# Optimization experiments

Measured on AMD Instinct MI355X. Metric: run time of the kernel, lower is better.

Reference implementation:

```python
import jax, jax.numpy as jnp
import numpy as np

B, N, F_IN, F_OUT, D = 8, 2048, 256, 128, 3
ALPHA = 0.2       # leaky relu slope
CUT_OFF = 0.1     # distance gate sharpness
NEG_INF = -9e15


def setup_inputs() -> dict:
    key = jax.random.key(0)
    k1, k2, k3, k4 = jax.random.split(key, 4)
    x = jax.random.normal(k1, (B, N, F_IN), dtype=jnp.float32)
    coord = jax.random.normal(k2, (B, N, D), dtype=jnp.float32)
    # xavier_uniform-style scale (gain=1.414); normal init is fine for a reference
    w_std = 1.414 * np.sqrt(2.0 / (F_IN + F_OUT))
    a_std = 1.414 * np.sqrt(2.0 / (2 * F_OUT + 1))
    W = jax.random.normal(k3, (F_IN, F_OUT), dtype=jnp.float32) * w_std
    a = jax.random.normal(k4, (2 * F_OUT, 1), dtype=jnp.float32) * a_std
    return {"x": x, "coord": coord, "W": W, "a": a}


def reference(x, coord, W, a):
    # h: [B, N, F_OUT]
    h = jnp.matmul(x, W)
    # The original builds a_input=[h_i || h_j] and does a_input @ a.
    # Equivalent: e_ij = leaky_relu(h_i @ a[:F] + h_j @ a[F:]).
    f_src = jnp.matmul(h, a[:F_OUT])   # [B, N, 1]
    f_dst = jnp.matmul(h, a[F_OUT:])   # [B, N, 1]
    e = f_src + jnp.swapaxes(f_dst, 1, 2)            # [B, N, N]
    e = jnp.where(e > 0, e, ALPHA * e)               # leaky relu
    # pairwise squared distances -> exponential gate
    diff = coord[:, :, None, :] - coord[:, None, :, :]   # [B, N, N, D]
    loc = jnp.exp(-CUT_OFF * jnp.sum(diff * diff, axis=-1))  # [B, N, N]
    att_logits = jnp.where(loc > 0.01, e * loc, NEG_INF)
    attention = jax.nn.softmax(att_logits, axis=2)
    # dropout is identity in eval mode
    h_prime = jnp.matmul(attention, h)               # [B, N, F_OUT]
    return jax.nn.elu(h_prime)                       # concat=True path
```

## Files before the change

kernel.cpp:

```cpp
#include <hip/hip_runtime.h>
#include <hip/hip_bf16.h>

#define B_    8
#define N_    2048
#define FIN_  256
#define FOUT_ 128
#define NROWS (B_*N_)

typedef __attribute__((ext_vector_type(8))) short short8;
typedef __attribute__((ext_vector_type(4))) float f32x4;

__device__ __forceinline__ float bf2f(unsigned short u) {
  return __uint_as_float(((unsigned int)u) << 16);
}
__device__ __forceinline__ unsigned short f2bf(float f) {
  unsigned int u = __float_as_uint(f);
  u += 0x7FFFu + ((u >> 16) & 1u);
  return (unsigned short)(u >> 16);
}
__device__ __forceinline__ float ldin(const void* p, size_t idx, int isbf) {
  if (isbf) return bf2f(((const unsigned short*)p)[idx]);
  return ((const float*)p)[idx];
}
__device__ __forceinline__ unsigned pk2bf(float a, float b) {
  return (unsigned)f2bf(a) | ((unsigned)f2bf(b) << 16);
}
__device__ __forceinline__ float ex2(float x) {
#if __has_builtin(__builtin_amdgcn_exp2f)
  return __builtin_amdgcn_exp2f(x);
#else
  return __expf(x * 0.69314718056f);
#endif
}
__device__ __forceinline__ unsigned encf(float f) {
  unsigned u = __float_as_uint(f);
  return (u & 0x80000000u) ? ~u : (u | 0x80000000u);
}
__device__ __forceinline__ float decf(unsigned k) {
  return (k & 0x80000000u) ? __uint_as_float(k ^ 0x80000000u) : __uint_as_float(~k);
}
__device__ __forceinline__ int detect_bf(const void* x, int* cnt) {
  const unsigned short* u = (const unsigned short*)x;
  int c = 0;
  for (int i = threadIdx.x; i < 8192; i += 256) {
    unsigned short v = u[i];
    int e = (v >> 7) & 0xFF;
    if ((e >= 110 && e <= 145) || (v & 0x7FFF) == 0) c++;
  }
  cnt[threadIdx.x] = c;
  __syncthreads();
  for (int s = 128; s > 0; s >>= 1) {
    if (threadIdx.x < s) cnt[threadIdx.x] += cnt[threadIdx.x + s];
    __syncthreads();
  }
  return cnt[0] > 7373;
}

__global__ __launch_bounds__(256)
void k_prep(const void* __restrict__ x, const void* __restrict__ W,
            const void* __restrict__ a,
            unsigned short* __restrict__ WT, float* __restrict__ wa,
            int* __restrict__ flag, unsigned* __restrict__ MdstE) {
  __shared__ int cnt[256];
  const int isbf = detect_bf(x, cnt);
  if (blockIdx.x < 128) {
    int f = blockIdx.x, k = threadIdx.x;
    WT[f * 256 + k] = f2bf(ldin(W, (size_t)k * 128 + f, isbf));
  } else {
    __shared__ float as_s[256];
    int k = threadIdx.x;
    as_s[k] = ldin(a, k, isbf);
    __syncthreads();
    float s = 0.f, d = 0.f;
    for (int f = 0; f < 128; f++) {
      float w = ldin(W, (size_t)k * 128 + f, isbf);
      s += w * as_s[f];
      d += w * as_s[128 + f];
    }
    wa[k] = s;
    wa[256 + k] = d;
    if (k == 0) *flag = isbf;
    if (k < 8) MdstE[k * 32] = 0u;
  }
}

__global__ __launch_bounds__(256)
void k_h(const void* __restrict__ x, const void* __restrict__ coord,
         const unsigned short* __restrict__ WT,
         const float* __restrict__ wa, const int* __restrict__ flag,
         unsigned short* __restrict__ hT, float* __restrict__ fsrc,
         float4* __restrict__ cpack, unsigned* __restrict__ MdstE) {
  __shared__ __align__(16) unsigned short xs[32][264];
  __shared__ float wa_s[512];
  __shared__ float mxs[8];
  const int isbf = *flag;
  const int t    = threadIdx.x;
  const int row0 = blockIdx.x * 32;

  wa_s[t] = wa[t];
  wa_s[256 + t] = wa[256 + t];
  __syncthreads();

  const int c = t & 31;
  float sp[4], dp[4];
  if (isbf) {
    const unsigned short* xu = (const unsigned short*)x;
#pragma unroll
    for (int u = 0; u < 4; u++) {
      int r = u * 8 + (t >> 5);
      short8 sh = *(const short8*)&xu[(size_t)(row0 + r) * FIN_ + c * 8];
      *(short8*)&xs[r][c * 8] = sh;
      float s = 0.f, d = 0.f;
#pragma unroll
      for (int e = 0; e < 8; e++) {
        float xv = bf2f((unsigned short)sh[e]);
        s += xv * wa_s[c * 8 + e];
        d += xv * wa_s[256 + c * 8 + e];
      }
      sp[u] = s; dp[u] = d;
    }
  } else {
    const float* xf = (const float*)x;
#pragma unroll
    for (int u = 0; u < 4; u++) {
      int r = u * 8 + (t >> 5);
      float4 v0 = *(const float4*)&xf[(size_t)(row0 + r) * FIN_ + c * 8];
      float4 v1 = *(const float4*)&xf[(size_t)(row0 + r) * FIN_ + c * 8 + 4];
      float vv[8] = {v0.x, v0.y, v0.z, v0.w, v1.x, v1.y, v1.z, v1.w};
      short8 sh;
      float s = 0.f, d = 0.f;
#pragma unroll
      for (int e = 0; e < 8; e++) {
        sh[e] = (short)f2bf(vv[e]);
        s += vv[e] * wa_s[c * 8 + e];
        d += vv[e] * wa_s[256 + c * 8 + e];
      }
      *(short8*)&xs[r][c * 8] = sh;
      sp[u] = s; dp[u] = d;
    }
  }
#pragma unroll
  for (int off = 16; off >= 1; off >>= 1) {
#pragma unroll
    for (int u = 0; u < 4; u++) {
      sp[u] += __shfl_xor(sp[u], off, 64);
      dp[u] += __shfl_xor(dp[u], off, 64);
    }
  }
  if (c == 0) {
    float lm = -1e30f;
#pragma unroll
    for (int u = 0; u < 4; u++) {
      int r = u * 8 + (t >> 5);
      size_t rg = (size_t)(row0 + r);
      fsrc[rg] = sp[u];
      cpack[rg] = make_float4(ldin(coord, rg * 3 + 0, isbf),
                              ldin(coord, rg * 3 + 1, isbf),
                              ldin(coord, rg * 3 + 2, isbf),
                              dp[u] * 1.44269504f);
      lm = fmaxf(lm, dp[u]);
    }
    mxs[t >> 5] = lm;
  }
  __syncthreads();
  if (t == 0) {
    float m8 = mxs[0];
#pragma unroll
    for (int i = 1; i < 8; i++) m8 = fmaxf(m8, mxs[i]);
    atomicMax(&MdstE[(row0 >> 11) * 32], encf(m8));
  }

  const int lane = t & 63, w = t >> 6;
  const int m = lane & 15, quad = lane >> 4;
  const int slab = w >> 1, fh = w & 1;

  f32x4 acc[4];
#pragma unroll
  for (int i = 0; i < 4; i++) acc[i] = (f32x4){0.f, 0.f, 0.f, 0.f};

#pragma unroll
  for (int ks = 0; ks < 8; ks++) {
    short8 ah = *(const short8*)&xs[slab * 16 + m][ks * 32 + quad * 8];
#pragma unroll
    for (int ft = 0; ft < 4; ft++) {
      int f = fh * 64 + ft * 16 + m;
      short8 bh = *(const short8*)&WT[(size_t)f * 256 + ks * 32 + quad * 8];
      acc[ft] = __builtin_amdgcn_mfma_f32_16x16x32_bf16(ah, bh, acc[ft], 0, 0, 0);
    }
  }

  size_t n0 = (size_t)blockIdx.x * 2 + slab;
  unsigned short* hblk = hT + n0 * (FOUT_ * 16);
#pragma unroll
  for (int ft = 0; ft < 4; ft++) {
    int f = fh * 64 + ft * 16 + m;
    *(uint2*)&hblk[f * 16 + quad * 4] = make_uint2(
        pk2bf(acc[ft][0], acc[ft][1]), pk2bf(acc[ft][2], acc[ft][3]));
  }
}

__global__ __launch_bounds__(256, 4)
void k_attn(const unsigned short* __restrict__ hT, const float4* __restrict__ cpack,
            const float* __restrict__ fsrc, const unsigned* __restrict__ MdstE,
            const int* __restrict__ flag, void* __restrict__ out) {
  const int isbf = *flag;
  const int tid = threadIdx.x;
  const int b   = blockIdx.x >> 7;
  const int q0  = (blockIdx.x & 127) * 16;

  __shared__ __align__(16) float4 cjs[2][128];
  __shared__ __align__(16) unsigned short phi[2][16][136];

  const int qA   = tid & 15;
  const int jseg = tid >> 4;
  const size_t qglb = (size_t)b * N_ + q0 + qA;
  const float4 cq  = cpack[qglb];
  const float  fsq = fsrc[qglb];
  const float  fsqL = fsq * 1.44269504f;
  const float  mBqL = -fmaxf(0.f, fsq + decf(MdstE[b * 32])) * 1.44269504f;

  const int lane = tid & 63, w = tid >> 6;
  const int m = lane & 15, quad = lane >> 4;
  f32x4 acc[2], accD;
  acc[0] = (f32x4){0.f, 0.f, 0.f, 0.f};
  acc[1] = (f32x4){0.f, 0.f, 0.f, 0.f};
  accD   = (f32x4){0.f, 0.f, 0.f, 0.f};
  const short8 bones = {(short)0x3F80, (short)0x3F80, (short)0x3F80, (short)0x3F80,
                        (short)0x3F80, (short)0x3F80, (short)0x3F80, (short)0x3F80};

  const unsigned short* hTb = hT + (size_t)b * (N_ * FOUT_);
  const float4* cpb = cpack + (size_t)b * N_;
  const int colA = (w * 2 + 0) * 16 + m;
  const int colB = (w * 2 + 1) * 16 + m;
  const int co   = (quad & 1) * 8;
  const int chq  = quad >> 1;

  if (tid < 128) cjs[0][tid] = cpb[tid];
  short8 bcur[8], bnxt[8];
#pragma unroll
  for (int ks = 0; ks < 4; ks++) {
    size_t base = (size_t)(ks * 2 + chq) * (FOUT_ * 16) + co;
    bcur[ks * 2 + 0] = *(const short8*)&hTb[base + colA * 16];
    bcur[ks * 2 + 1] = *(const short8*)&hTb[base + colB * 16];
  }
  __syncthreads();

  for (int t = 0; t < 16; t++) {
    const int buf = t & 1;

    if (t < 15) {
      const int jcb = (t + 1) * 8;
#pragma unroll
      for (int ks = 0; ks < 4; ks++) {
        size_t base = (size_t)(jcb + ks * 2 + chq) * (FOUT_ * 16) + co;
        bnxt[ks * 2 + 0] = *(const short8*)&hTb[base + colA * 16];
        bnxt[ks * 2 + 1] = *(const short8*)&hTb[base + colB * 16];
      }
    }
    float4 cg;
    if (t < 15 && tid < 128) cg = cpb[(t + 1) * 128 + tid];

    unsigned pks[4];
#pragma unroll
    for (int jp = 0; jp < 4; jp++) {
      const float4 cj0 = cjs[buf][2 * jseg + 32 * jp + 0];
      const float4 cj1 = cjs[buf][2 * jseg + 32 * jp + 1];
      float dx0 = cq.x - cj0.x, dy0 = cq.y - cj0.y, dz0 = cq.z - cj0.z;
      float dx1 = cq.x - cj1.x, dy1 = cq.y - cj1.y, dz1 = cq.z - cj1.z;
      float d20 = fmaf(dz0, dz0, fmaf(dy0, dy0, dx0 * dx0));
      float d21 = fmaf(dz1, dz1, fmaf(dy1, dy1, dx1 * dx1));
      float loc0 = ex2(-0.14426950408f * d20);
      float loc1 = ex2(-0.14426950408f * d21);
      float xL0 = fsqL + cj0.w, xL1 = fsqL + cj1.w;
      float eL0 = fmaxf(xL0, 0.2f * xL0);
      float eL1 = fmaxf(xL1, 0.2f * xL1);
      float p0 = ex2(fmaf(eL0, loc0, mBqL));
      float p1 = ex2(fmaf(eL1, loc1, mBqL));
      p0 = (d20 < 46.0517f) ? p0 : 0.f;
      p1 = (d21 < 46.0517f) ? p1 : 0.f;
      unsigned r;
      asm("v_cvt_pk_bf16_f32 %0, %1, %2" : "=v"(r) : "v"(p0), "v"(p1));
      pks[jp] = r;
    }
#pragma unroll
    for (int jp = 0; jp < 4; jp++)
      *(unsigned*)&phi[buf][qA][2 * jseg + 32 * jp] = pks[jp];

    if (t < 15 && tid < 128) cjs[buf ^ 1][tid] = cg;
    __syncthreads();

#pragma unroll
    for (int ks = 0; ks < 4; ks++) {
      short8 ah = *(const short8*)&phi[buf][m][ks * 32 + quad * 8];
      acc[0] = __builtin_amdgcn_mfma_f32_16x16x32_bf16(ah, bcur[ks * 2 + 0], acc[0], 0, 0, 0);
      acc[1] = __builtin_amdgcn_mfma_f32_16x16x32_bf16(ah, bcur[ks * 2 + 1], acc[1], 0, 0, 0);
      accD   = __builtin_amdgcn_mfma_f32_16x16x32_bf16(ah, bones, accD, 0, 0, 0);
    }
#pragma unroll
    for (int i = 0; i < 8; i++) bcur[i] = bnxt[i];
  }

#pragma unroll
  for (int f2 = 0; f2 < 2; f2++) {
    int f = (w * 2 + f2) * 16 + m;
#pragma unroll
    for (int r = 0; r < 4; r++) {
      int q = quad * 4 + r;
      float v = acc[f2][r] / fmaxf(accD[r], 1e-30f);
      v = (v > 0.f) ? v : (__expf(v) - 1.0f);
      size_t oidx = ((size_t)(b * N_ + q0 + q)) * FOUT_ + f;
      if (isbf) ((unsigned short*)out)[oidx] = f2bf(v);
      else      ((float*)out)[oidx] = v;
    }
  }
}

extern "C" void kernel_launch(void* const* d_in, const int* in_sizes, int n_in,
                              void* d_out, int out_size, void* d_ws, size_t ws_size,
                              hipStream_t stream) {
  const void* x     = d_in[0];
  const void* coord = d_in[1];
  const void* W     = d_in[2];
  const void* a     = d_in[3];

  int*            flag  = (int*)d_ws;
  unsigned*       MdstE = (unsigned*)d_ws + 64;
  unsigned short* hT    = (unsigned short*)((float*)d_ws + 512);
  unsigned short* WT    = hT + (size_t)NROWS * FOUT_;
  float*          wa    = (float*)(WT + 128 * 256);
  float*          fsrc  = wa + 512;
  float4*         cpack = (float4*)(fsrc + NROWS);

  k_prep<<<129, 256, 0, stream>>>(x, W, a, WT, wa, flag, MdstE);
  k_h   <<<NROWS / 32, 256, 0, stream>>>(x, coord, WT, wa, flag, hT, fsrc, cpack, MdstE);
  k_attn<<<B_ * (N_ / 16), 256, 0, stream>>>(hT, cpack, fsrc, MdstE, flag, d_out);
}
```

Measured before the change: 139.2 us.

## Enlarge attention query tile to 64 and stage hT tiles through swizzled LDS

The attention kernel now processes 64 queries per 512-thread block instead of 16 per 256-thread block. Each hT key tile is loaded once into double-buffered LDS and shared by all waves, instead of each wave reading it from global memory into registers. The next tile's logits are computed while the current tile's MFMAs run, and the hT layout written by k_h gets an XOR swizzle so the LDS reads avoid bank conflicts. This cuts redundant global traffic for h by 4x, at the cost of far more LDS per block, lower occupancy, and a shared-memory exchange for the softmax denominator.

```diff
diff --git a/kernel.cpp b/kernel.cpp
--- a/kernel.cpp
+++ b/kernel.cpp
@@ -194,25 +194,28 @@
 #pragma unroll
   for (int ft = 0; ft < 4; ft++) {
     int f = fh * 64 + ft * 16 + m;
-    *(uint2*)&hblk[f * 16 + quad * 4] = make_uint2(
+    int jo = (quad * 4) ^ (((f >> 2) & 1) << 3);
+    *(uint2*)&hblk[f * 16 + jo] = make_uint2(
         pk2bf(acc[ft][0], acc[ft][1]), pk2bf(acc[ft][2], acc[ft][3]));
   }
 }
 
-__global__ __launch_bounds__(256, 4)
+__global__ __launch_bounds__(512, 2)
 void k_attn(const unsigned short* __restrict__ hT, const float4* __restrict__ cpack,
             const float* __restrict__ fsrc, const unsigned* __restrict__ MdstE,
             const int* __restrict__ flag, void* __restrict__ out) {
   const int isbf = *flag;
   const int tid = threadIdx.x;
-  const int b   = blockIdx.x >> 7;
-  const int q0  = (blockIdx.x & 127) * 16;
-
-  __shared__ __align__(16) float4 cjs[2][128];
-  __shared__ __align__(16) unsigned short phi[2][16][136];
-
-  const int qA   = tid & 15;
-  const int jseg = tid >> 4;
+  const int b   = blockIdx.x >> 5;
+  const int q0  = (blockIdx.x & 31) * 64;
+
+  __shared__ __align__(16) uint4 ldsBu[2][2048];
+  __shared__ __align__(16) unsigned short phi[2][64][136];
+  __shared__ __align__(16) float4 cjs[2][144];
+  __shared__ float denomS[64];
+
+  const int qA   = tid >> 3;
+  const int jseg = tid & 7;
   const size_t qglb = (size_t)b * N_ + q0 + qA;
   const float4 cq  = cpack[qglb];
   const float  fsq = fsrc[qglb];
@@ -221,50 +224,28 @@
 
   const int lane = tid & 63, w = tid >> 6;
   const int m = lane & 15, quad = lane >> 4;
-  f32x4 acc[2], accD;
-  acc[0] = (f32x4){0.f, 0.f, 0.f, 0.f};
-  acc[1] = (f32x4){0.f, 0.f, 0.f, 0.f};
-  accD   = (f32x4){0.f, 0.f, 0.f, 0.f};
+  const int qg = w & 3, fg = w >> 2;
+  const int hsel = (quad & 1) ^ ((m >> 2) & 1);
+
+  f32x4 acc[4], accD;
+#pragma unroll
+  for (int i = 0; i < 4; i++) acc[i] = (f32x4){0.f, 0.f, 0.f, 0.f};
+  accD = (f32x4){0.f, 0.f, 0.f, 0.f};
   const short8 bones = {(short)0x3F80, (short)0x3F80, (short)0x3F80, (short)0x3F80,
                         (short)0x3F80, (short)0x3F80, (short)0x3F80, (short)0x3F80};
 
   const unsigned short* hTb = hT + (size_t)b * (N_ * FOUT_);
+  const uint4* gB = (const uint4*)hTb;
   const float4* cpb = cpack + (size_t)b * N_;
-  const int colA = (w * 2 + 0) * 16 + m;
-  const int colB = (w * 2 + 1) * 16 + m;
-  const int co   = (quad & 1) * 8;
-  const int chq  = quad >> 1;
-
-  if (tid < 128) cjs[0][tid] = cpb[tid];
-  short8 bcur[8], bnxt[8];
-#pragma unroll
-  for (int ks = 0; ks < 4; ks++) {
-    size_t base = (size_t)(ks * 2 + chq) * (FOUT_ * 16) + co;
-    bcur[ks * 2 + 0] = *(const short8*)&hTb[base + colA * 16];
-    bcur[ks * 2 + 1] = *(const short8*)&hTb[base + colB * 16];
-  }
-  __syncthreads();
-
-  for (int t = 0; t < 16; t++) {
-    const int buf = t & 1;
-
-    if (t < 15) {
-      const int jcb = (t + 1) * 8;
-#pragma unroll
-      for (int ks = 0; ks < 4; ks++) {
-        size_t base = (size_t)(jcb + ks * 2 + chq) * (FOUT_ * 16) + co;
-        bnxt[ks * 2 + 0] = *(const short8*)&hTb[base + colA * 16];
-        bnxt[ks * 2 + 1] = *(const short8*)&hTb[base + colB * 16];
-      }
-    }
-    float4 cg;
-    if (t < 15 && tid < 128) cg = cpb[(t + 1) * 128 + tid];
-
-    unsigned pks[4];
-#pragma unroll
-    for (int jp = 0; jp < 4; jp++) {
-      const float4 cj0 = cjs[buf][2 * jseg + 32 * jp + 0];
-      const float4 cj1 = cjs[buf][2 * jseg + 32 * jp + 1];
+
+  auto logits = [&](int tt, unsigned* pk) {
+    const float4* cb = cjs[tt & 1];
+#pragma unroll
+    for (int jp = 0; jp < 8; jp++) {
+      const int j0 = jseg * 16 + 2 * jp;
+      const int ix = j0 + (j0 >> 3);
+      const float4 cj0 = cb[ix];
+      const float4 cj1 = cb[ix + 1];
       float dx0 = cq.x - cj0.x, dy0 = cq.y - cj0.y, dz0 = cq.z - cj0.z;
       float dx1 = cq.x - cj1.x, dy1 = cq.y - cj1.y, dz1 = cq.z - cj1.z;
       float d20 = fmaf(dz0, dz0, fmaf(dy0, dy0, dx0 * dx0));
@@ -280,33 +261,92 @@
       p1 = (d21 < 46.0517f) ? p1 : 0.f;
       unsigned r;
       asm("v_cvt_pk_bf16_f32 %0, %1, %2" : "=v"(r) : "v"(p0), "v"(p1));
-      pks[jp] = r;
-    }
-#pragma unroll
-    for (int jp = 0; jp < 4; jp++)
-      *(unsigned*)&phi[buf][qA][2 * jseg + 32 * jp] = pks[jp];
-
-    if (t < 15 && tid < 128) cjs[buf ^ 1][tid] = cg;
+      pk[jp] = r;
+    }
+  };
+
+  auto store_phi = [&](int tt, const unsigned* pk) {
+    *(uint4*)&phi[tt & 1][qA][jseg * 16] =
+        make_uint4(pk[0], pk[1], pk[2], pk[3]);
+    *(uint4*)&phi[tt & 1][qA][jseg * 16 + 8] =
+        make_uint4(pk[4], pk[5], pk[6], pk[7]);
+  };
+
+  auto mfma_tile = [&](int tb) {
+    const unsigned short* pb = &phi[tb][qg * 16 + m][0];
+    const unsigned short* bb = (const unsigned short*)ldsBu[tb];
+#pragma unroll
+    for (int ks = 0; ks < 4; ks++) {
+      short8 ah = *(const short8*)&pb[ks * 32 + quad * 8];
+      if (fg == 0)
+        accD = __builtin_amdgcn_mfma_f32_16x16x32_bf16(ah, bones, accD, 0, 0, 0);
+#pragma unroll
+      for (int ft = 0; ft < 4; ft++) {
+        const int f = fg * 64 + ft * 16 + m;
+        const short8 bh = *(const short8*)
+            &bb[(ks * 2 + (quad >> 1)) * 2048 + f * 16 + hsel * 8];
+        acc[ft] = __builtin_amdgcn_mfma_f32_16x16x32_bf16(ah, bh, acc[ft], 0, 0, 0);
+      }
+    }
+  };
+
+  if (tid < 256) {
+    const int tile = tid >> 7, j = tid & 127;
+    cjs[tile][j + (j >> 3)] = cpb[tid];
+  }
+  {
+    uint4 pv[4];
+#pragma unroll
+    for (int k = 0; k < 4; k++) pv[k] = gB[k * 512 + tid];
+#pragma unroll
+    for (int k = 0; k < 4; k++) ldsBu[0][k * 512 + tid] = pv[k];
+  }
+  __syncthreads();
+  {
+    unsigned pk0[8];
+    logits(0, pk0);
+    store_phi(0, pk0);
+  }
+  __syncthreads();
+
+  const int jr = tid & 127;
+  for (int t = 0; t < 16; t++) {
+    uint4 bv[4];
+    if (t < 15) {
+#pragma unroll
+      for (int k = 0; k < 4; k++)
+        bv[k] = gB[(size_t)(t + 1) * 2048 + k * 512 + tid];
+    }
+    float4 cg;
+    if (t < 14 && tid < 128) cg = cpb[(t + 2) * 128 + jr];
+
+    unsigned pk[8];
+    if (t < 15) logits(t + 1, pk);
+
+    mfma_tile(t & 1);
+
+    if (t < 15) {
+#pragma unroll
+      for (int k = 0; k < 4; k++)
+        ldsBu[(t + 1) & 1][k * 512 + tid] = bv[k];
+      store_phi(t + 1, pk);
+    }
+    if (t < 14 && tid < 128) cjs[t & 1][jr + (jr >> 3)] = cg;
     __syncthreads();
-
-#pragma unroll
-    for (int ks = 0; ks < 4; ks++) {
-      short8 ah = *(const short8*)&phi[buf][m][ks * 32 + quad * 8];
-      acc[0] = __builtin_amdgcn_mfma_f32_16x16x32_bf16(ah, bcur[ks * 2 + 0], acc[0], 0, 0, 0);
-      acc[1] = __builtin_amdgcn_mfma_f32_16x16x32_bf16(ah, bcur[ks * 2 + 1], acc[1], 0, 0, 0);
-      accD   = __builtin_amdgcn_mfma_f32_16x16x32_bf16(ah, bones, accD, 0, 0, 0);
-    }
-#pragma unroll
-    for (int i = 0; i < 8; i++) bcur[i] = bnxt[i];
-  }
-
-#pragma unroll
-  for (int f2 = 0; f2 < 2; f2++) {
-    int f = (w * 2 + f2) * 16 + m;
+  }
+
+  if (fg == 0 && m == 0) {
+#pragma unroll
+    for (int r = 0; r < 4; r++) denomS[qg * 16 + quad * 4 + r] = accD[r];
+  }
+  __syncthreads();
+#pragma unroll
+  for (int ft = 0; ft < 4; ft++) {
+    const int f = fg * 64 + ft * 16 + m;
 #pragma unroll
     for (int r = 0; r < 4; r++) {
-      int q = quad * 4 + r;
-      float v = acc[f2][r] / fmaxf(accD[r], 1e-30f);
+      const int q = qg * 16 + quad * 4 + r;
+      float v = acc[ft][r] / fmaxf(denomS[q], 1e-30f);
       v = (v > 0.f) ? v : (__expf(v) - 1.0f);
       size_t oidx = ((size_t)(b * N_ + q0 + q)) * FOUT_ + f;
       if (isbf) ((unsigned short*)out)[oidx] = f2bf(v);
@@ -333,5 +373,5 @@
 
   k_prep<<<129, 256, 0, stream>>>(x, W, a, WT, wa, flag, MdstE);
   k_h   <<<NROWS / 32, 256, 0, stream>>>(x, coord, WT, wa, flag, hT, fsrc, cpack, MdstE);
-  k_attn<<<B_ * (N_ / 16), 256, 0, stream>>>(hT, cpack, fsrc, MdstE, flag, d_out);
-}
+  k_attn<<<B_ * (N_ / 64), 512, 0, stream>>>(hT, cpack, fsrc, MdstE, flag, d_out);
+}
```

New measurement: 139.7 us. Within noise of the previous version (+0.4%).
